# Optimization experiments

Hardware: AMD Instinct MI355X
Metric: run time of the kernel (lower is better)

Reference implementation:

```python
import jax, jax.numpy as jnp
import numpy as np

B = 64          # graphs per batch
MAX_NODES = 512 # nodes per graph
N = B * MAX_NODES
DEG = 16
E = N * DEG
F_IN = 12
H, D = 4, 32    # heads, per-head dim
HID = H * D     # 128
A = 512         # num_outputs (action space)
NEG_SLOPE = 0.2


def setup_inputs() -> dict:
    key = jax.random.key(0)
    ks = jax.random.split(key, 32)
    x = jax.random.normal(ks[0], (N, F_IN), dtype=jnp.float32)
    # edges confined within each graph's node block (as in the torch adjacency loop)
    src_l = jax.random.randint(ks[1], (B, MAX_NODES * DEG), 0, MAX_NODES, dtype=jnp.int32)
    dst_l = jax.random.randint(ks[2], (B, MAX_NODES * DEG), 0, MAX_NODES, dtype=jnp.int32)
    offs = (jnp.arange(B, dtype=jnp.int32) * MAX_NODES)[:, None]
    edge_src = (src_l + offs).reshape(-1)
    edge_dst = (dst_l + offs).reshape(-1)
    batch_idx = jnp.repeat(jnp.arange(B, dtype=jnp.int32), MAX_NODES)

    s = 0.1
    p = {}
    p["Wl0"] = s * jax.random.normal(ks[3], (F_IN, H, D), dtype=jnp.float32)
    p["Wr0"] = s * jax.random.normal(ks[4], (F_IN, H, D), dtype=jnp.float32)
    p["att0"] = s * jax.random.normal(ks[5], (H, D), dtype=jnp.float32)
    p["b0"] = jnp.zeros((HID,), dtype=jnp.float32)
    p["Wl"] = s * jax.random.normal(ks[6], (3, HID, H, D), dtype=jnp.float32)
    p["Wr"] = s * jax.random.normal(ks[7], (3, HID, H, D), dtype=jnp.float32)
    p["att"] = s * jax.random.normal(ks[8], (3, H, D), dtype=jnp.float32)
    p["b"] = jnp.zeros((3, HID), dtype=jnp.float32)
    p["qW1"] = s * jax.random.normal(ks[9], (2 * HID, HID), dtype=jnp.float32)
    p["qb1"] = jnp.zeros((HID,), dtype=jnp.float32)
    p["qW2"] = s * jax.random.normal(ks[10], (HID, A), dtype=jnp.float32)
    p["qb2"] = jnp.zeros((A,), dtype=jnp.float32)
    p["vW1"] = s * jax.random.normal(ks[11], (2 * HID, HID), dtype=jnp.float32)
    p["vb1"] = jnp.zeros((HID,), dtype=jnp.float32)
    p["vW2"] = s * jax.random.normal(ks[12], (HID, 1), dtype=jnp.float32)
    p["vb2"] = jnp.zeros((1,), dtype=jnp.float32)
    return dict(x=x, edge_src=edge_src, edge_dst=edge_dst, batch_idx=batch_idx, **p)


def _gatv2(x, src, dst, Wl, Wr, att, b):
    n = x.shape[0]
    xl = jnp.einsum('nf,fhd->nhd', x, Wl)  # source transform [N,H,D]
    xr = jnp.einsum('nf,fhd->nhd', x, Wr)  # target transform [N,H,D]
    xj = xl[src]                            # [E,H,D]
    e = jax.nn.leaky_relu(xj + xr[dst], NEG_SLOPE)
    s = jnp.einsum('ehd,hd->eh', e, att)    # [E,H]
    smax = jax.ops.segment_max(s, dst, num_segments=n)
    smax = jnp.where(jnp.isfinite(smax), smax, 0.0)
    a = jnp.exp(s - smax[dst])
    den = jax.ops.segment_sum(a, dst, num_segments=n)
    a = a / jnp.maximum(den[dst], 1e-16)
    out = jax.ops.segment_sum(a[:, :, None] * xj, dst, num_segments=n)  # [N,H,D]
    return out.reshape(n, H * D) + b


def reference(x, edge_src, edge_dst, batch_idx,
              Wl0, Wr0, att0, b0, Wl, Wr, att, b,
              qW1, qb1, qW2, qb2, vW1, vb1, vW2, vb2):
    h = jax.nn.relu(_gatv2(x, edge_src, edge_dst, Wl0, Wr0, att0, b0))
    for i in range(3):  # remaining num_layers-1 GATv2 layers (dropout off in eval)
        h = jax.nn.relu(_gatv2(h, edge_src, edge_dst, Wl[i], Wr[i], att[i], b[i]))
    nb = h.shape[0] // MAX_NODES
    gsum = jax.ops.segment_sum(h, batch_idx, num_segments=nb)
    cnt = jax.ops.segment_sum(jnp.ones((h.shape[0], 1), h.dtype), batch_idx, num_segments=nb)
    gmean = gsum / jnp.maximum(cnt, 1.0)
    gmax = jax.ops.segment_max(h, batch_idx, num_segments=nb)
    g = jnp.concatenate([gmean, gmax], axis=-1)  # [B, 2*HID]
    adv = jax.nn.relu(g @ qW1 + qb1) @ qW2 + qb2
    val = jax.nn.relu(g @ vW1 + vb1) @ vW2 + vb2
    q = val + (adv - adv.mean(axis=-1, keepdims=True))
    return q
```

## Files before the change

### kernel.cpp

```cpp
#include <hip/hip_runtime.h>
#include <hip/hip_bf16.h>

#define NN 32768
#define EE 524288
#define HID 128
#define BGRAPH 64
#define MAXN 512
#define AOUT 512
#define MAXDEG 64

typedef __attribute__((ext_vector_type(8))) short short8;
typedef __attribute__((ext_vector_type(4))) float f32x4;
typedef unsigned short ushort;
typedef unsigned int uint;

__device__ __forceinline__ ushort bf16_rn(float f) {
    uint u = __float_as_uint(f);
    u += 0x7FFF + ((u >> 16) & 1);
    return (ushort)(u >> 16);
}
__device__ __forceinline__ void bf16_split(float f, ushort& hi, ushort& lo) {
    hi = bf16_rn(f);
    float fh = __uint_as_float(((uint)hi) << 16);
    lo = bf16_rn(f - fh);
}

__device__ __forceinline__ float vsum4(f32x4 v) {
    return (v.x + v.y) + (v.z + v.w);
}

__global__ __launch_bounds__(256) void setup_kernel(
    const int* __restrict__ src, const int* __restrict__ dst,
    int* __restrict__ cursor, int* __restrict__ bucket,
    const float* __restrict__ Wl, const float* __restrict__ Wr,
    ushort* __restrict__ wt_hi, ushort* __restrict__ wt_lo) {
    int blk = blockIdx.x;
    if (blk < EE / 256) {
        int i = blk * 256 + threadIdx.x;
        int d = dst[i];
        int p = atomicAdd(&cursor[d], 1);
        if (p < MAXDEG) bucket[(size_t)d * MAXDEG + p] = src[i];
    } else {
        int idx = (blk - EE / 256) * 256 + threadIdx.x;
        if (idx >= 98304) return;
        int c = idx & 127;
        int k = (idx >> 7) & 127;
        int l = (idx >> 14) % 3;
        int lr = idx / 49152;
        float v = (lr ? Wr : Wl)[l * 16384 + k * 128 + c];
        ushort hi, lo;
        bf16_split(v, hi, lo);
        int ct = c >> 4, m = c & 15;
        int ks = k >> 5;
        int lane = (((k >> 3) & 3) << 4) | m;
        int j = k & 7;
        size_t o = ((size_t)(lr * 3 + l) * 32 + ct * 4 + ks) * 512 + lane * 8 + j;
        wt_hi[o] = hi;
        wt_lo[o] = lo;
    }
}

template<int KTOT, int KC>
__global__ __launch_bounds__(256) void transform3(
    const float* __restrict__ hin, const float* __restrict__ Wl,
    const float* __restrict__ Wr, float* __restrict__ xl, float* __restrict__ xr) {
    __shared__ float wb[KC][256];
    __shared__ float ha[KC][36];
    int b = blockIdx.x;
    int xcd = b & 7, slot = b >> 3;
    int graph = xcd + 8 * (slot >> 4);
    int chunk = slot & 15;
    int node0 = graph * 512 + chunk * 32;
    int t = threadIdx.x;
    int c32 = t & 31;
    int ng  = t >> 5;
    const float4* wl4g = (const float4*)Wl;
    const float4* wr4g = (const float4*)Wr;
    for (int idx = t; idx < KC * 64; idx += 256) {
        int k = idx >> 6, r = idx & 63;
        float4 v = (r < 32) ? wl4g[k * 32 + r] : wr4g[k * 32 + (r - 32)];
        ((float4*)&wb[k][0])[r] = v;
    }
    for (int idx = t; idx < 32 * KC; idx += 256) {
        int m = idx / KC, kk = idx - m * KC;
        ha[kk][m] = hin[(size_t)(node0 + m) * KTOT + kk];
    }
    __syncthreads();
    float4 accL[4], accR[4];
#pragma unroll
    for (int m = 0; m < 4; m++) {
        accL[m].x = accL[m].y = accL[m].z = accL[m].w = 0.f;
        accR[m].x = accR[m].y = accR[m].z = accR[m].w = 0.f;
    }
#pragma unroll
    for (int kk = 0; kk < KC; kk++) {
        float4 wl = ((const float4*)&wb[kk][0])[c32];
        float4 wr = ((const float4*)&wb[kk][128])[c32];
        float4 hv = *(const float4*)&ha[kk][ng * 4];
        accL[0].x = fmaf(hv.x, wl.x, accL[0].x); accL[0].y = fmaf(hv.x, wl.y, accL[0].y);
        accL[0].z = fmaf(hv.x, wl.z, accL[0].z); accL[0].w = fmaf(hv.x, wl.w, accL[0].w);
        accL[1].x = fmaf(hv.y, wl.x, accL[1].x); accL[1].y = fmaf(hv.y, wl.y, accL[1].y);
        accL[1].z = fmaf(hv.y, wl.z, accL[1].z); accL[1].w = fmaf(hv.y, wl.w, accL[1].w);
        accL[2].x = fmaf(hv.z, wl.x, accL[2].x); accL[2].y = fmaf(hv.z, wl.y, accL[2].y);
        accL[2].z = fmaf(hv.z, wl.z, accL[2].z); accL[2].w = fmaf(hv.z, wl.w, accL[2].w);
        accL[3].x = fmaf(hv.w, wl.x, accL[3].x); accL[3].y = fmaf(hv.w, wl.y, accL[3].y);
        accL[3].z = fmaf(hv.w, wl.z, accL[3].z); accL[3].w = fmaf(hv.w, wl.w, accL[3].w);
        accR[0].x = fmaf(hv.x, wr.x, accR[0].x); accR[0].y = fmaf(hv.x, wr.y, accR[0].y);
        accR[0].z = fmaf(hv.x, wr.z, accR[0].z); accR[0].w = fmaf(hv.x, wr.w, accR[0].w);
        accR[1].x = fmaf(hv.y, wr.x, accR[1].x); accR[1].y = fmaf(hv.y, wr.y, accR[1].y);
        accR[1].z = fmaf(hv.y, wr.z, accR[1].z); accR[1].w = fmaf(hv.y, wr.w, accR[1].w);
        accR[2].x = fmaf(hv.z, wr.x, accR[2].x); accR[2].y = fmaf(hv.z, wr.y, accR[2].y);
        accR[2].z = fmaf(hv.z, wr.z, accR[2].z); accR[2].w = fmaf(hv.z, wr.w, accR[2].w);
        accR[3].x = fmaf(hv.w, wr.x, accR[3].x); accR[3].y = fmaf(hv.w, wr.y, accR[3].y);
        accR[3].z = fmaf(hv.w, wr.z, accR[3].z); accR[3].w = fmaf(hv.w, wr.w, accR[3].w);
    }
    float4* xlo = (float4*)xl;
    float4* xro = (float4*)xr;
#pragma unroll
    for (int m = 0; m < 4; m++) {
        int n = node0 + ng * 4 + m;
        xlo[n * 32 + c32] = accL[m];
        xro[n * 32 + c32] = accR[m];
    }
}

__device__ __forceinline__ void gat_node2_dual(
    const f32x4* __restrict__ xl4, const f32x4* __restrict__ xr4,
    const int* __restrict__ browA, int nEA, int nA,
    const int* __restrict__ browB, int nEB, int nBn,
    int el2, int p16, f32x4 at0, f32x4 at1,
    f32x4& oA0, f32x4& oA1, f32x4& oB0, f32x4& oB1) {
    f32x4 xrA0 = xr4[(size_t)nA * 32 + p16 * 2];
    f32x4 xrA1 = xr4[(size_t)nA * 32 + p16 * 2 + 1];
    f32x4 xrB0 = xr4[(size_t)nBn * 32 + p16 * 2];
    f32x4 xrB1 = xr4[(size_t)nBn * 32 + p16 * 2 + 1];
    f32x4 aA0 = {0.f, 0.f, 0.f, 0.f};
    f32x4 aA1 = {0.f, 0.f, 0.f, 0.f};
    f32x4 aB0 = {0.f, 0.f, 0.f, 0.f};
    f32x4 aB1 = {0.f, 0.f, 0.f, 0.f};
    float denA = 0.f, denB = 0.f;
    int nBlkA = (nEA + 7) >> 3;
    int nBlkB = (nEB + 7) >> 3;
    int nBlk = nBlkA > nBlkB ? nBlkA : nBlkB;
    int4 iA = *(const int4*)(browA + el2 * 4);
    int4 iB = *(const int4*)(browB + el2 * 4);
    for (int blk = 0; blk < nBlk; blk++) {
        int ebase = blk * 8 + el2 * 4;
        int noff = ebase + 8;
        int nmax = MAXDEG - 8 + el2 * 4;
        noff = noff > nmax ? nmax : noff;
        int4 iAn = *(const int4*)(browA + noff);
        int4 iBn = *(const int4*)(browB + noff);

#define LOADC(c, vA0_, vA1_, vB0_, vB1_) {                                        \
        int rawA = (c == 0) ? iA.x : (c == 1) ? iA.y : (c == 2) ? iA.z : iA.w;    \
        int rawB = (c == 0) ? iB.x : (c == 1) ? iB.y : (c == 2) ? iB.z : iB.w;    \
        int e = ebase + c;                                                        \
        int sA = (e < nEA) ? rawA : nA;                                           \
        int sB = (e < nEB) ? rawB : nBn;                                          \
        const f32x4* rA = xl4 + (size_t)sA * 32 + p16 * 2;                        \
        const f32x4* rB = xl4 + (size_t)sB * 32 + p16 * 2;                        \
        vA0_ = rA[0]; vA1_ = rA[1]; vB0_ = rB[0]; vB1_ = rB[1]; }

#define COMPUTEC(c, vA0_, vA1_, vB0_, vB1_) {                                     \
        int e = ebase + c;                                                        \
        f32x4 u, lA0, lA1, lB0, lB1;                                              \
        u = vA0_ + xrA0; lA0 = __builtin_elementwise_max(u, 0.2f * u);            \
        u = vA1_ + xrA1; lA1 = __builtin_elementwise_max(u, 0.2f * u);            \
        u = vB0_ + xrB0; lB0 = __builtin_elementwise_max(u, 0.2f * u);            \
        u = vB1_ + xrB1; lB1 = __builtin_elementwise_max(u, 0.2f * u);            \
        f32x4 tvA = at0 * lA0 + at1 * lA1;                                        \
        f32x4 tvB = at0 * lB0 + at1 * lB1;                                        \
        float tA = vsum4(tvA), tB = vsum4(tvB);                                   \
        tA += __shfl_xor(tA, 1); tA += __shfl_xor(tA, 2);                         \
        tB += __shfl_xor(tB, 1); tB += __shfl_xor(tB, 2);                         \
        float wA = (e < nEA) ? __expf(tA) : 0.f;                                  \
        float wB = (e < nEB) ? __expf(tB) : 0.f;                                  \
        denA += wA; denB += wB;                                                   \
        aA0 += wA * vA0_; aA1 += wA * vA1_;                                       \
        aB0 += wB * vB0_; aB1 += wB * vB1_; }

        f32x4 p0, p1, p2, p3, q0, q1, q2, q3;
        LOADC(0, p0, p1, p2, p3)
        LOADC(1, q0, q1, q2, q3)
        COMPUTEC(0, p0, p1, p2, p3)
        LOADC(2, p0, p1, p2, p3)
        COMPUTEC(1, q0, q1, q2, q3)
        LOADC(3, q0, q1, q2, q3)
        COMPUTEC(2, p0, p1, p2, p3)
        COMPUTEC(3, q0, q1, q2, q3)
#undef LOADC
#undef COMPUTEC
        iA = iAn; iB = iBn;
    }
    aA0.x += __shfl_xor(aA0.x, 16); aA0.y += __shfl_xor(aA0.y, 16);
    aA0.z += __shfl_xor(aA0.z, 16); aA0.w += __shfl_xor(aA0.w, 16);
    aA1.x += __shfl_xor(aA1.x, 16); aA1.y += __shfl_xor(aA1.y, 16);
    aA1.z += __shfl_xor(aA1.z, 16); aA1.w += __shfl_xor(aA1.w, 16);
    aB0.x += __shfl_xor(aB0.x, 16); aB0.y += __shfl_xor(aB0.y, 16);
    aB0.z += __shfl_xor(aB0.z, 16); aB0.w += __shfl_xor(aB0.w, 16);
    aB1.x += __shfl_xor(aB1.x, 16); aB1.y += __shfl_xor(aB1.y, 16);
    aB1.z += __shfl_xor(aB1.z, 16); aB1.w += __shfl_xor(aB1.w, 16);
    denA += __shfl_xor(denA, 16);
    denB += __shfl_xor(denB, 16);
    float rdenA = 1.0f / fmaxf(denA, 1e-16f);
    float rdenB = 1.0f / fmaxf(denB, 1e-16f);
    oA0 = aA0 * rdenA; oA1 = aA1 * rdenA;
    oB0 = aB0 * rdenB; oB1 = aB1 * rdenB;
}

__device__ __forceinline__ f32x4 relu_bias(f32x4 o, f32x4 bv) {
    f32x4 z = {0.f, 0.f, 0.f, 0.f};
    return __builtin_elementwise_max(o + bv, z);
}

__device__ __forceinline__ void store_h(f32x4 o0, f32x4 o1,
                                        ushort (*hh)[136], ushort (*hl)[136],
                                        int nl, int p16) {
    float f[8];
    f[0] = o0.x; f[1] = o0.y; f[2] = o0.z; f[3] = o0.w;
    f[4] = o1.x; f[5] = o1.y; f[6] = o1.z; f[7] = o1.w;
    ushort hi[8], lo[8];
#pragma unroll
    for (int i = 0; i < 8; i++) bf16_split(f[i], hi[i], lo[i]);
    uint4 ph, pl;
    ph.x = (uint)hi[0] | ((uint)hi[1] << 16);
    ph.y = (uint)hi[2] | ((uint)hi[3] << 16);
    ph.z = (uint)hi[4] | ((uint)hi[5] << 16);
    ph.w = (uint)hi[6] | ((uint)hi[7] << 16);
    pl.x = (uint)lo[0] | ((uint)lo[1] << 16);
    pl.y = (uint)lo[2] | ((uint)lo[3] << 16);
    pl.z = (uint)lo[4] | ((uint)lo[5] << 16);
    pl.w = (uint)lo[6] | ((uint)lo[7] << 16);
    *(uint4*)&hh[nl][p16 * 8] = ph;
    *(uint4*)&hl[nl][p16 * 8] = pl;
}

__global__ __launch_bounds__(256, 4) void fused_agg_mfma(
    const float* __restrict__ xl_in, const float* __restrict__ xr_in,
    const int* __restrict__ bucket, const int* __restrict__ cnt,
    const float* __restrict__ att, const float* __restrict__ bias,
    const ushort* __restrict__ wl_hi, const ushort* __restrict__ wl_lo,
    const ushort* __restrict__ wr_hi, const ushort* __restrict__ wr_lo,
    float* __restrict__ xl_out, float* __restrict__ xr_out) {
    __shared__ ushort hh[16][136];
    __shared__ ushort hl[16][136];
    int b = blockIdx.x;
    int xcd = b & 7, slot = b >> 3;
    int graph = xcd + 8 * (slot >> 5);
    int chunk = slot & 31;
    int node_base = graph * 512 + chunk * 16;
    int wid = threadIdx.x >> 6;
    int lane = threadIdx.x & 63;
    int n0 = node_base + wid * 4;
    int nh  = lane >> 5;
    int el2 = (lane >> 4) & 1;
    int p16 = lane & 15;
    {
        const f32x4* xl4 = (const f32x4*)xl_in;
        const f32x4* xr4 = (const f32x4*)xr_in;
        const f32x4* att4 = (const f32x4*)att;
        f32x4 at0 = att4[p16 * 2];
        f32x4 at1 = att4[p16 * 2 + 1];
        int nA  = n0 + nh;
        int nBn = n0 + 2 + nh;
        int nEA = cnt[nA];  nEA = (nEA > MAXDEG) ? MAXDEG : nEA;
        int nEB = cnt[nBn]; nEB = (nEB > MAXDEG) ? MAXDEG : nEB;
        f32x4 oA0, oA1, oB0, oB1;
        gat_node2_dual(xl4, xr4,
                       bucket + (size_t)nA * MAXDEG, nEA, nA,
                       bucket + (size_t)nBn * MAXDEG, nEB, nBn,
                       el2, p16, at0, at1, oA0, oA1, oB0, oB1);
        if (el2 == 0) {
            const f32x4* bias4 = (const f32x4*)bias;
            f32x4 b0v = bias4[p16 * 2];
            f32x4 b1v = bias4[p16 * 2 + 1];
            oA0 = relu_bias(oA0, b0v); oA1 = relu_bias(oA1, b1v);
            oB0 = relu_bias(oB0, b0v); oB1 = relu_bias(oB1, b1v);
            store_h(oA0, oA1, hh, hl, wid * 4 + nh, p16);
            store_h(oB0, oB1, hh, hl, wid * 4 + 2 + nh, p16);
        }
    }
    __syncthreads();
    int m = lane & 15, quad = lane >> 4;
    f32x4 accL[2], accR[2];
#pragma unroll
    for (int c2 = 0; c2 < 2; c2++) {
        accL[c2] = (f32x4){0.f, 0.f, 0.f, 0.f};
        accR[c2] = (f32x4){0.f, 0.f, 0.f, 0.f};
    }
#pragma unroll
    for (int ks = 0; ks < 4; ks++) {
        short8 ah = *(const short8*)&hh[m][ks * 32 + quad * 8];
        short8 al = *(const short8*)&hl[m][ks * 32 + quad * 8];
#pragma unroll
        for (int c2 = 0; c2 < 2; c2++) {
            int ct = wid * 2 + c2;
            size_t wb = ((size_t)(ct * 4 + ks) * 64 + lane) * 8;
            short8 bhl = *(const short8*)(wl_hi + wb);
            short8 bll = *(const short8*)(wl_lo + wb);
            short8 bhr = *(const short8*)(wr_hi + wb);
            short8 blr = *(const short8*)(wr_lo + wb);
            accL[c2] = __builtin_amdgcn_mfma_f32_16x16x32_bf16(ah, bhl, accL[c2], 0, 0, 0);
            accL[c2] = __builtin_amdgcn_mfma_f32_16x16x32_bf16(ah, bll, accL[c2], 0, 0, 0);
            accL[c2] = __builtin_amdgcn_mfma_f32_16x16x32_bf16(al, bhl, accL[c2], 0, 0, 0);
            accR[c2] = __builtin_amdgcn_mfma_f32_16x16x32_bf16(ah, bhr, accR[c2], 0, 0, 0);
            accR[c2] = __builtin_amdgcn_mfma_f32_16x16x32_bf16(ah, blr, accR[c2], 0, 0, 0);
            accR[c2] = __builtin_amdgcn_mfma_f32_16x16x32_bf16(al, bhr, accR[c2], 0, 0, 0);
        }
    }
#pragma unroll
    for (int c2 = 0; c2 < 2; c2++) {
        int ct = wid * 2 + c2;
#pragma unroll
        for (int r = 0; r < 4; r++) {
            int node = node_base + quad * 4 + r;
            xl_out[(size_t)node * 128 + ct * 16 + m] = accL[c2][r];
            xr_out[(size_t)node * 128 + ct * 16 + m] = accR[c2][r];
        }
    }
}

__global__ __launch_bounds__(256, 4) void agg_pool(
    const float* __restrict__ xl_in, const float* __restrict__ xr_in,
    const int* __restrict__ bucket, const int* __restrict__ cnt,
    const float* __restrict__ att, const float* __restrict__ bias,
    float* __restrict__ psum, float* __restrict__ pmax) {
    __shared__ float sums[4][128];
    __shared__ float maxs[4][128];
    int b = blockIdx.x;
    int xcd = b & 7, slot = b >> 3;
    int graph = xcd + 8 * (slot >> 5);
    int chunk = slot & 31;
    int wid = threadIdx.x >> 6;
    int lane = threadIdx.x & 63;
    int n0 = graph * 512 + chunk * 16 + wid * 4;
    int nh  = lane >> 5;
    int el2 = (lane >> 4) & 1;
    int p16 = lane & 15;
    const f32x4* xl4 = (const f32x4*)xl_in;
    const f32x4* xr4 = (const f32x4*)xr_in;
    const f32x4* att4 = (const f32x4*)att;
    const f32x4* bias4 = (const f32x4*)bias;
    f32x4 at0 = att4[p16 * 2];
    f32x4 at1 = att4[p16 * 2 + 1];
    f32x4 b0v = bias4[p16 * 2];
    f32x4 b1v = bias4[p16 * 2 + 1];
    int nA  = n0 + nh;
    int nBn = n0 + 2 + nh;
    int nEA = cnt[nA];  nEA = (nEA > MAXDEG) ? MAXDEG : nEA;
    int nEB = cnt[nBn]; nEB = (nEB > MAXDEG) ? MAXDEG : nEB;
    f32x4 oA0, oA1, oB0, oB1;
    gat_node2_dual(xl4, xr4,
                   bucket + (size_t)nA * MAXDEG, nEA, nA,
                   bucket + (size_t)nBn * MAXDEG, nEB, nBn,
                   el2, p16, at0, at1, oA0, oA1, oB0, oB1);
    oA0 = relu_bias(oA0, b0v); oA1 = relu_bias(oA1, b1v);
    oB0 = relu_bias(oB0, b0v); oB1 = relu_bias(oB1, b1v);
    f32x4 s0 = oA0 + oB0;
    f32x4 s1 = oA1 + oB1;
    f32x4 m0 = __builtin_elementwise_max(oA0, oB0);
    f32x4 m1 = __builtin_elementwise_max(oA1, oB1);
    s0.x += __shfl_xor(s0.x, 32); s0.y += __shfl_xor(s0.y, 32);
    s0.z += __shfl_xor(s0.z, 32); s0.w += __shfl_xor(s0.w, 32);
    s1.x += __shfl_xor(s1.x, 32); s1.y += __shfl_xor(s1.y, 32);
    s1.z += __shfl_xor(s1.z, 32); s1.w += __shfl_xor(s1.w, 32);
    m0.x = fmaxf(m0.x, __shfl_xor(m0.x, 32)); m0.y = fmaxf(m0.y, __shfl_xor(m0.y, 32));
    m0.z = fmaxf(m0.z, __shfl_xor(m0.z, 32)); m0.w = fmaxf(m0.w, __shfl_xor(m0.w, 32));
    m1.x = fmaxf(m1.x, __shfl_xor(m1.x, 32)); m1.y = fmaxf(m1.y, __shfl_xor(m1.y, 32));
    m1.z = fmaxf(m1.z, __shfl_xor(m1.z, 32)); m1.w = fmaxf(m1.w, __shfl_xor(m1.w, 32));
    if (nh == 0 && el2 == 0) {
        *(f32x4*)&sums[wid][p16 * 8]     = s0;
        *(f32x4*)&sums[wid][p16 * 8 + 4] = s1;
        *(f32x4*)&maxs[wid][p16 * 8]     = m0;
        *(f32x4*)&maxs[wid][p16 * 8 + 4] = m1;
    }
    __syncthreads();
    int t = threadIdx.x;
    if (t < 128) {
        float s = 0.f, m = -1e30f;
#pragma unroll
        for (int ww = 0; ww < 4; ww++) {
            s += sums[ww][t];
            m = fmaxf(m, maxs[ww][t]);
        }
        psum[((size_t)graph * 32 + chunk) * 128 + t] = s;
        pmax[((size_t)graph * 32 + chunk) * 128 + t] = m;
    }
}

__global__ __launch_bounds__(512) void head_kernel(
    const float* __restrict__ psum, const float* __restrict__ pmax,
    const float* __restrict__ qW1, const float* __restrict__ qb1,
    const float* __restrict__ qW2, const float* __restrict__ qb2,
    const float* __restrict__ vW1, const float* __restrict__ vb1,
    const float* __restrict__ vW2, const float* __restrict__ vb2,
    float* __restrict__ qout) {
    __shared__ float gs[256];
    __shared__ float hq[128];
    __shared__ float hv[128];
    __shared__ float red[512];
    int b = blockIdx.x, t = threadIdx.x;
    if (t < 128) {
        float s = 0.f, m = -1e30f;
#pragma unroll 8
        for (int c = 0; c < 32; c++) {
            s += psum[((size_t)b * 32 + c) * 128 + t];
            m = fmaxf(m, pmax[((size_t)b * 32 + c) * 128 + t]);
        }
        gs[t] = s * (1.0f / 512.0f);
        gs[128 + t] = m;
    }
    __syncthreads();
    if (t < 128) {
        float acc = qb1[t];
        for (int k = 0; k < 256; k++) acc = fmaf(gs[k], qW1[k * 128 + t], acc);
        hq[t] = fmaxf(acc, 0.f);
    } else if (t < 256) {
        int tt = t - 128;
        float acc = vb1[tt];
        for (int k = 0; k < 256; k++) acc = fmaf(gs[k], vW1[k * 128 + tt], acc);
        hv[tt] = fmaxf(acc, 0.f);
    }
    __syncthreads();
    float adv = qb2[t];
    for (int k = 0; k < 128; k++) adv = fmaf(hq[k], qW2[k * 512 + t], adv);
    red[t] = (t < 128) ? hv[t] * vW2[t] : 0.f;
    __syncthreads();
    for (int off = 256; off > 0; off >>= 1) {
        if (t < off) red[t] += red[t + off];
        __syncthreads();
    }
    float val = red[0] + vb2[0];
    __syncthreads();
    red[t] = adv;
    __syncthreads();
    for (int off = 256; off > 0; off >>= 1) {
        if (t < off) red[t] += red[t + off];
        __syncthreads();
    }
    float mean_adv = red[0] * (1.0f / 512.0f);
    qout[b * 512 + t] = val + adv - mean_adv;
}

extern "C" void kernel_launch(void* const* d_in, const int* in_sizes, int n_in,
                              void* d_out, int out_size, void* d_ws, size_t ws_size,
                              hipStream_t stream) {
    const float* x        = (const float*)d_in[0];
    const int* edge_src   = (const int*)d_in[1];
    const int* edge_dst   = (const int*)d_in[2];
    const float* Wl0 = (const float*)d_in[4];
    const float* Wr0 = (const float*)d_in[5];
    const float* att0 = (const float*)d_in[6];
    const float* b0 = (const float*)d_in[7];
    const float* Wl = (const float*)d_in[8];
    const float* Wr = (const float*)d_in[9];
    const float* att = (const float*)d_in[10];
    const float* bb = (const float*)d_in[11];
    const float* qW1 = (const float*)d_in[12];
    const float* qb1 = (const float*)d_in[13];
    const float* qW2 = (const float*)d_in[14];
    const float* qb2 = (const float*)d_in[15];
    const float* vW1 = (const float*)d_in[16];
    const float* vb1 = (const float*)d_in[17];
    const float* vW2 = (const float*)d_in[18];
    const float* vb2 = (const float*)d_in[19];

    int* cursor  = (int*)d_ws;
    int* bucket  = cursor + NN;
    float* fbase = (float*)(bucket + (size_t)NN * MAXDEG);
    float* xlA   = fbase;
    float* xrA   = xlA + NN * 128;
    float* xlB   = xrA + NN * 128;
    float* xrB   = xlB + NN * 128;
    float* psum  = xrB + NN * 128;
    float* pmax  = psum + BGRAPH * 32 * 128;
    ushort* wthi = (ushort*)(pmax + BGRAPH * 32 * 128);
    ushort* wtlo = wthi + 2 * 3 * 16384;

    hipMemsetAsync(cursor, 0, NN * sizeof(int), stream);
    setup_kernel<<<EE / 256 + 384, 256, 0, stream>>>(edge_src, edge_dst, cursor, bucket,
                                                     Wl, Wr, wthi, wtlo);

    transform3<12, 12><<<NN / 32, 256, 0, stream>>>(x, Wl0, Wr0, xlA, xrA);

    fused_agg_mfma<<<NN / 16, 256, 0, stream>>>(xlA, xrA, bucket, cursor, att0, b0,
                                                wthi + 0 * 16384, wtlo + 0 * 16384,
                                                wthi + 3 * 16384, wtlo + 3 * 16384,
                                                xlB, xrB);
    fused_agg_mfma<<<NN / 16, 256, 0, stream>>>(xlB, xrB, bucket, cursor, att, bb,
                                                wthi + 1 * 16384, wtlo + 1 * 16384,
                                                wthi + 4 * 16384, wtlo + 4 * 16384,
                                                xlA, xrA);
    fused_agg_mfma<<<NN / 16, 256, 0, stream>>>(xlA, xrA, bucket, cursor,
                                                att + 128, bb + 128,
                                                wthi + 2 * 16384, wtlo + 2 * 16384,
                                                wthi + 5 * 16384, wtlo + 5 * 16384,
                                                xlB, xrB);
    agg_pool<<<NN / 16, 256, 0, stream>>>(xlB, xrB, bucket, cursor,
                                          att + 256, bb + 256, psum, pmax);
    head_kernel<<<BGRAPH, 512, 0, stream>>>(psum, pmax, qW1, qb1, qW2, qb2,
                                            vW1, vb1, vW2, vb2, (float*)d_out);
}
```

Before: 271.3 us.

## Split each node's edge list across four lane groups with 512-thread blocks

Each wave now aggregates two nodes instead of four, and the 64 lanes split each node's edges into four interleaved groups of 4 (16 edges per iteration) instead of two. Blocks grow to 512 threads (8 waves per 16 nodes), and each wave in the MFMA projection handles one 16-column tile instead of two. The aim is more memory-level parallelism and shorter per-wave edge loops for the gather-bound aggregation. The cost is an extra cross-lane reduction step, more padding waste for low-degree nodes with 16-edge blocks, and higher register pressure under launch_bounds(512,4).

```diff
diff --git a/kernel.cpp b/kernel.cpp
--- a/kernel.cpp
+++ b/kernel.cpp
@@ -128,7 +128,7 @@
     const f32x4* __restrict__ xl4, const f32x4* __restrict__ xr4,
     const int* __restrict__ browA, int nEA, int nA,
     const int* __restrict__ browB, int nEB, int nBn,
-    int el2, int p16, f32x4 at0, f32x4 at1,
+    int el4, int p16, f32x4 at0, f32x4 at1,
     f32x4& oA0, f32x4& oA1, f32x4& oB0, f32x4& oB1) {
     f32x4 xrA0 = xr4[(size_t)nA * 32 + p16 * 2];
     f32x4 xrA1 = xr4[(size_t)nA * 32 + p16 * 2 + 1];
@@ -139,15 +139,14 @@
     f32x4 aB0 = {0.f, 0.f, 0.f, 0.f};
     f32x4 aB1 = {0.f, 0.f, 0.f, 0.f};
     float denA = 0.f, denB = 0.f;
-    int nBlkA = (nEA + 7) >> 3;
-    int nBlkB = (nEB + 7) >> 3;
-    int nBlk = nBlkA > nBlkB ? nBlkA : nBlkB;
-    int4 iA = *(const int4*)(browA + el2 * 4);
-    int4 iB = *(const int4*)(browB + el2 * 4);
+    int nEmax = nEA > nEB ? nEA : nEB;
+    int nBlk = (nEmax + 15) >> 4;
+    int4 iA = *(const int4*)(browA + el4 * 4);
+    int4 iB = *(const int4*)(browB + el4 * 4);
     for (int blk = 0; blk < nBlk; blk++) {
-        int ebase = blk * 8 + el2 * 4;
-        int noff = ebase + 8;
-        int nmax = MAXDEG - 8 + el2 * 4;
+        int ebase = blk * 16 + el4 * 4;
+        int noff = ebase + 16;
+        int nmax = (MAXDEG - 16) + el4 * 4;
         noff = noff > nmax ? nmax : noff;
         int4 iAn = *(const int4*)(browA + noff);
         int4 iBn = *(const int4*)(browB + noff);
@@ -193,16 +192,17 @@
 #undef COMPUTEC
         iA = iAn; iB = iBn;
     }
-    aA0.x += __shfl_xor(aA0.x, 16); aA0.y += __shfl_xor(aA0.y, 16);
-    aA0.z += __shfl_xor(aA0.z, 16); aA0.w += __shfl_xor(aA0.w, 16);
-    aA1.x += __shfl_xor(aA1.x, 16); aA1.y += __shfl_xor(aA1.y, 16);
-    aA1.z += __shfl_xor(aA1.z, 16); aA1.w += __shfl_xor(aA1.w, 16);
-    aB0.x += __shfl_xor(aB0.x, 16); aB0.y += __shfl_xor(aB0.y, 16);
-    aB0.z += __shfl_xor(aB0.z, 16); aB0.w += __shfl_xor(aB0.w, 16);
-    aB1.x += __shfl_xor(aB1.x, 16); aB1.y += __shfl_xor(aB1.y, 16);
-    aB1.z += __shfl_xor(aB1.z, 16); aB1.w += __shfl_xor(aB1.w, 16);
+#define RED16_32(v) \
+    v.x += __shfl_xor(v.x, 16); v.y += __shfl_xor(v.y, 16);                      \
+    v.z += __shfl_xor(v.z, 16); v.w += __shfl_xor(v.w, 16);                      \
+    v.x += __shfl_xor(v.x, 32); v.y += __shfl_xor(v.y, 32);                      \
+    v.z += __shfl_xor(v.z, 32); v.w += __shfl_xor(v.w, 32);
+    RED16_32(aA0) RED16_32(aA1) RED16_32(aB0) RED16_32(aB1)
+#undef RED16_32
     denA += __shfl_xor(denA, 16);
+    denA += __shfl_xor(denA, 32);
     denB += __shfl_xor(denB, 16);
+    denB += __shfl_xor(denB, 32);
     float rdenA = 1.0f / fmaxf(denA, 1e-16f);
     float rdenB = 1.0f / fmaxf(denB, 1e-16f);
     oA0 = aA0 * rdenA; oA1 = aA1 * rdenA;
@@ -236,7 +236,7 @@
     *(uint4*)&hl[nl][p16 * 8] = pl;
 }
 
-__global__ __launch_bounds__(256, 4) void fused_agg_mfma(
+__global__ __launch_bounds__(512, 4) void fused_agg_mfma(
     const float* __restrict__ xl_in, const float* __restrict__ xr_in,
     const int* __restrict__ bucket, const int* __restrict__ cnt,
     const float* __restrict__ att, const float* __restrict__ bias,
@@ -252,9 +252,7 @@
     int node_base = graph * 512 + chunk * 16;
     int wid = threadIdx.x >> 6;
     int lane = threadIdx.x & 63;
-    int n0 = node_base + wid * 4;
-    int nh  = lane >> 5;
-    int el2 = (lane >> 4) & 1;
+    int el4 = (lane >> 4) & 3;
     int p16 = lane & 15;
     {
         const f32x4* xl4 = (const f32x4*)xl_in;
@@ -262,81 +260,68 @@
         const f32x4* att4 = (const f32x4*)att;
         f32x4 at0 = att4[p16 * 2];
         f32x4 at1 = att4[p16 * 2 + 1];
-        int nA  = n0 + nh;
-        int nBn = n0 + 2 + nh;
+        int nA  = node_base + wid * 2;
+        int nBn = node_base + wid * 2 + 1;
         int nEA = cnt[nA];  nEA = (nEA > MAXDEG) ? MAXDEG : nEA;
         int nEB = cnt[nBn]; nEB = (nEB > MAXDEG) ? MAXDEG : nEB;
         f32x4 oA0, oA1, oB0, oB1;
         gat_node2_dual(xl4, xr4,
                        bucket + (size_t)nA * MAXDEG, nEA, nA,
                        bucket + (size_t)nBn * MAXDEG, nEB, nBn,
-                       el2, p16, at0, at1, oA0, oA1, oB0, oB1);
-        if (el2 == 0) {
+                       el4, p16, at0, at1, oA0, oA1, oB0, oB1);
+        if (el4 == 0) {
             const f32x4* bias4 = (const f32x4*)bias;
             f32x4 b0v = bias4[p16 * 2];
             f32x4 b1v = bias4[p16 * 2 + 1];
             oA0 = relu_bias(oA0, b0v); oA1 = relu_bias(oA1, b1v);
             oB0 = relu_bias(oB0, b0v); oB1 = relu_bias(oB1, b1v);
-            store_h(oA0, oA1, hh, hl, wid * 4 + nh, p16);
-            store_h(oB0, oB1, hh, hl, wid * 4 + 2 + nh, p16);
+            store_h(oA0, oA1, hh, hl, wid * 2, p16);
+            store_h(oB0, oB1, hh, hl, wid * 2 + 1, p16);
         }
     }
     __syncthreads();
     int m = lane & 15, quad = lane >> 4;
-    f32x4 accL[2], accR[2];
-#pragma unroll
-    for (int c2 = 0; c2 < 2; c2++) {
-        accL[c2] = (f32x4){0.f, 0.f, 0.f, 0.f};
-        accR[c2] = (f32x4){0.f, 0.f, 0.f, 0.f};
-    }
+    f32x4 accL = {0.f, 0.f, 0.f, 0.f};
+    f32x4 accR = {0.f, 0.f, 0.f, 0.f};
+    int ct = wid;
 #pragma unroll
     for (int ks = 0; ks < 4; ks++) {
         short8 ah = *(const short8*)&hh[m][ks * 32 + quad * 8];
         short8 al = *(const short8*)&hl[m][ks * 32 + quad * 8];
-#pragma unroll
-        for (int c2 = 0; c2 < 2; c2++) {
-            int ct = wid * 2 + c2;
-            size_t wb = ((size_t)(ct * 4 + ks) * 64 + lane) * 8;
-            short8 bhl = *(const short8*)(wl_hi + wb);
-            short8 bll = *(const short8*)(wl_lo + wb);
-            short8 bhr = *(const short8*)(wr_hi + wb);
-            short8 blr = *(const short8*)(wr_lo + wb);
-            accL[c2] = __builtin_amdgcn_mfma_f32_16x16x32_bf16(ah, bhl, accL[c2], 0, 0, 0);
-            accL[c2] = __builtin_amdgcn_mfma_f32_16x16x32_bf16(ah, bll, accL[c2], 0, 0, 0);
-            accL[c2] = __builtin_amdgcn_mfma_f32_16x16x32_bf16(al, bhl, accL[c2], 0, 0, 0);
-            accR[c2] = __builtin_amdgcn_mfma_f32_16x16x32_bf16(ah, bhr, accR[c2], 0, 0, 0);
-            accR[c2] = __builtin_amdgcn_mfma_f32_16x16x32_bf16(ah, blr, accR[c2], 0, 0, 0);
-            accR[c2] = __builtin_amdgcn_mfma_f32_16x16x32_bf16(al, bhr, accR[c2], 0, 0, 0);
-        }
-    }
-#pragma unroll
-    for (int c2 = 0; c2 < 2; c2++) {
-        int ct = wid * 2 + c2;
-#pragma unroll
-        for (int r = 0; r < 4; r++) {
-            int node = node_base + quad * 4 + r;
-            xl_out[(size_t)node * 128 + ct * 16 + m] = accL[c2][r];
-            xr_out[(size_t)node * 128 + ct * 16 + m] = accR[c2][r];
-        }
-    }
-}
-
-__global__ __launch_bounds__(256, 4) void agg_pool(
+        size_t wb = ((size_t)(ct * 4 + ks) * 64 + lane) * 8;
+        short8 bhl = *(const short8*)(wl_hi + wb);
+        short8 bll = *(const short8*)(wl_lo + wb);
+        short8 bhr = *(const short8*)(wr_hi + wb);
+        short8 blr = *(const short8*)(wr_lo + wb);
+        accL = __builtin_amdgcn_mfma_f32_16x16x32_bf16(ah, bhl, accL, 0, 0, 0);
+        accL = __builtin_amdgcn_mfma_f32_16x16x32_bf16(ah, bll, accL, 0, 0, 0);
+        accL = __builtin_amdgcn_mfma_f32_16x16x32_bf16(al, bhl, accL, 0, 0, 0);
+        accR = __builtin_amdgcn_mfma_f32_16x16x32_bf16(ah, bhr, accR, 0, 0, 0);
+        accR = __builtin_amdgcn_mfma_f32_16x16x32_bf16(ah, blr, accR, 0, 0, 0);
+        accR = __builtin_amdgcn_mfma_f32_16x16x32_bf16(al, bhr, accR, 0, 0, 0);
+    }
+#pragma unroll
+    for (int r = 0; r < 4; r++) {
+        int node = node_base + quad * 4 + r;
+        xl_out[(size_t)node * 128 + ct * 16 + m] = accL[r];
+        xr_out[(size_t)node * 128 + ct * 16 + m] = accR[r];
+    }
+}
+
+__global__ __launch_bounds__(512, 4) void agg_pool(
     const float* __restrict__ xl_in, const float* __restrict__ xr_in,
     const int* __restrict__ bucket, const int* __restrict__ cnt,
     const float* __restrict__ att, const float* __restrict__ bias,
     float* __restrict__ psum, float* __restrict__ pmax) {
-    __shared__ float sums[4][128];
-    __shared__ float maxs[4][128];
+    __shared__ float sums[8][128];
+    __shared__ float maxs[8][128];
     int b = blockIdx.x;
     int xcd = b & 7, slot = b >> 3;
     int graph = xcd + 8 * (slot >> 5);
     int chunk = slot & 31;
     int wid = threadIdx.x >> 6;
     int lane = threadIdx.x & 63;
-    int n0 = graph * 512 + chunk * 16 + wid * 4;
-    int nh  = lane >> 5;
-    int el2 = (lane >> 4) & 1;
+    int el4 = (lane >> 4) & 3;
     int p16 = lane & 15;
     const f32x4* xl4 = (const f32x4*)xl_in;
     const f32x4* xr4 = (const f32x4*)xr_in;
@@ -346,30 +331,23 @@
     f32x4 at1 = att4[p16 * 2 + 1];
     f32x4 b0v = bias4[p16 * 2];
     f32x4 b1v = bias4[p16 * 2 + 1];
-    int nA  = n0 + nh;
-    int nBn = n0 + 2 + nh;
+    int node_base = graph * 512 + chunk * 16;
+    int nA  = node_base + wid * 2;
+    int nBn = node_base + wid * 2 + 1;
     int nEA = cnt[nA];  nEA = (nEA > MAXDEG) ? MAXDEG : nEA;
     int nEB = cnt[nBn]; nEB = (nEB > MAXDEG) ? MAXDEG : nEB;
     f32x4 oA0, oA1, oB0, oB1;
     gat_node2_dual(xl4, xr4,
                    bucket + (size_t)nA * MAXDEG, nEA, nA,
                    bucket + (size_t)nBn * MAXDEG, nEB, nBn,
-                   el2, p16, at0, at1, oA0, oA1, oB0, oB1);
+                   el4, p16, at0, at1, oA0, oA1, oB0, oB1);
     oA0 = relu_bias(oA0, b0v); oA1 = relu_bias(oA1, b1v);
     oB0 = relu_bias(oB0, b0v); oB1 = relu_bias(oB1, b1v);
     f32x4 s0 = oA0 + oB0;
     f32x4 s1 = oA1 + oB1;
     f32x4 m0 = __builtin_elementwise_max(oA0, oB0);
     f32x4 m1 = __builtin_elementwise_max(oA1, oB1);
-    s0.x += __shfl_xor(s0.x, 32); s0.y += __shfl_xor(s0.y, 32);
-    s0.z += __shfl_xor(s0.z, 32); s0.w += __shfl_xor(s0.w, 32);
-    s1.x += __shfl_xor(s1.x, 32); s1.y += __shfl_xor(s1.y, 32);
-    s1.z += __shfl_xor(s1.z, 32); s1.w += __shfl_xor(s1.w, 32);
-    m0.x = fmaxf(m0.x, __shfl_xor(m0.x, 32)); m0.y = fmaxf(m0.y, __shfl_xor(m0.y, 32));
-    m0.z = fmaxf(m0.z, __shfl_xor(m0.z, 32)); m0.w = fmaxf(m0.w, __shfl_xor(m0.w, 32));
-    m1.x = fmaxf(m1.x, __shfl_xor(m1.x, 32)); m1.y = fmaxf(m1.y, __shfl_xor(m1.y, 32));
-    m1.z = fmaxf(m1.z, __shfl_xor(m1.z, 32)); m1.w = fmaxf(m1.w, __shfl_xor(m1.w, 32));
-    if (nh == 0 && el2 == 0) {
+    if (el4 == 0) {
         *(f32x4*)&sums[wid][p16 * 8]     = s0;
         *(f32x4*)&sums[wid][p16 * 8 + 4] = s1;
         *(f32x4*)&maxs[wid][p16 * 8]     = m0;
@@ -380,7 +358,7 @@
     if (t < 128) {
         float s = 0.f, m = -1e30f;
 #pragma unroll
-        for (int ww = 0; ww < 4; ww++) {
+        for (int ww = 0; ww < 8; ww++) {
             s += sums[ww][t];
             m = fmaxf(m, maxs[ww][t]);
         }
@@ -484,20 +462,20 @@
 
     transform3<12, 12><<<NN / 32, 256, 0, stream>>>(x, Wl0, Wr0, xlA, xrA);
 
-    fused_agg_mfma<<<NN / 16, 256, 0, stream>>>(xlA, xrA, bucket, cursor, att0, b0,
+    fused_agg_mfma<<<NN / 16, 512, 0, stream>>>(xlA, xrA, bucket, cursor, att0, b0,
                                                 wthi + 0 * 16384, wtlo + 0 * 16384,
                                                 wthi + 3 * 16384, wtlo + 3 * 16384,
                                                 xlB, xrB);
-    fused_agg_mfma<<<NN / 16, 256, 0, stream>>>(xlB, xrB, bucket, cursor, att, bb,
+    fused_agg_mfma<<<NN / 16, 512, 0, stream>>>(xlB, xrB, bucket, cursor, att, bb,
                                                 wthi + 1 * 16384, wtlo + 1 * 16384,
                                                 wthi + 4 * 16384, wtlo + 4 * 16384,
                                                 xlA, xrA);
-    fused_agg_mfma<<<NN / 16, 256, 0, stream>>>(xlA, xrA, bucket, cursor,
+    fused_agg_mfma<<<NN / 16, 512, 0, stream>>>(xlA, xrA, bucket, cursor,
                                                 att + 128, bb + 128,
                                                 wthi + 2 * 16384, wtlo + 2 * 16384,
                                                 wthi + 5 * 16384, wtlo + 5 * 16384,
                                                 xlB, xrB);
-    agg_pool<<<NN / 16, 256, 0, stream>>>(xlB, xrB, bucket, cursor,
+    agg_pool<<<NN / 16, 512, 0, stream>>>(xlB, xrB, bucket, cursor,
                                           att + 256, bb + 256, psum, pmax);
     head_kernel<<<BGRAPH, 512, 0, stream>>>(psum, pmax, qW1, qb1, qW2, qb2,
                                             vW1, vb1, vW2, vb2, (float*)d_out);
```

Result: slower. 287.6 us (+6.0%).

## Process one node per wave with four edge lanes instead of dual-node pairs

Applied to the files above, without the earlier changes.

Replaces the dual-node aggregation, where each wave handled two node pairs with two edge slots, with a per-node loop in which all 64 lanes work on one node at a time: four edge groups of 16 lanes, with a one-ahead prefetch of the next gathered row. Each wave now loops serially over its four nodes. The aim is to cut wasted iterations when degrees differ between paired nodes (the old loop ran to the max of the two) and to lower register pressure. The trade-off is less memory-level parallelism per wave, since fewer independent gathers are in flight and the node loop is serialized.

```diff
diff --git a/kernel.cpp b/kernel.cpp
--- a/kernel.cpp
+++ b/kernel.cpp
@@ -124,89 +124,55 @@
     }
 }
 
-__device__ __forceinline__ void gat_node2_dual(
-    const f32x4* __restrict__ xl4, const f32x4* __restrict__ xr4,
-    const int* __restrict__ browA, int nEA, int nA,
-    const int* __restrict__ browB, int nEB, int nBn,
-    int el2, int p16, f32x4 at0, f32x4 at1,
-    f32x4& oA0, f32x4& oA1, f32x4& oB0, f32x4& oB1) {
-    f32x4 xrA0 = xr4[(size_t)nA * 32 + p16 * 2];
-    f32x4 xrA1 = xr4[(size_t)nA * 32 + p16 * 2 + 1];
-    f32x4 xrB0 = xr4[(size_t)nBn * 32 + p16 * 2];
-    f32x4 xrB1 = xr4[(size_t)nBn * 32 + p16 * 2 + 1];
-    f32x4 aA0 = {0.f, 0.f, 0.f, 0.f};
-    f32x4 aA1 = {0.f, 0.f, 0.f, 0.f};
-    f32x4 aB0 = {0.f, 0.f, 0.f, 0.f};
-    f32x4 aB1 = {0.f, 0.f, 0.f, 0.f};
-    float denA = 0.f, denB = 0.f;
-    int nBlkA = (nEA + 7) >> 3;
-    int nBlkB = (nEB + 7) >> 3;
-    int nBlk = nBlkA > nBlkB ? nBlkA : nBlkB;
-    int4 iA = *(const int4*)(browA + el2 * 4);
-    int4 iB = *(const int4*)(browB + el2 * 4);
-    for (int blk = 0; blk < nBlk; blk++) {
-        int ebase = blk * 8 + el2 * 4;
-        int noff = ebase + 8;
-        int nmax = MAXDEG - 8 + el2 * 4;
-        noff = noff > nmax ? nmax : noff;
-        int4 iAn = *(const int4*)(browA + noff);
-        int4 iBn = *(const int4*)(browB + noff);
-
-#define LOADC(c, vA0_, vA1_, vB0_, vB1_) {                                        \
-        int rawA = (c == 0) ? iA.x : (c == 1) ? iA.y : (c == 2) ? iA.z : iA.w;    \
-        int rawB = (c == 0) ? iB.x : (c == 1) ? iB.y : (c == 2) ? iB.z : iB.w;    \
-        int e = ebase + c;                                                        \
-        int sA = (e < nEA) ? rawA : nA;                                           \
-        int sB = (e < nEB) ? rawB : nBn;                                          \
-        const f32x4* rA = xl4 + (size_t)sA * 32 + p16 * 2;                        \
-        const f32x4* rB = xl4 + (size_t)sB * 32 + p16 * 2;                        \
-        vA0_ = rA[0]; vA1_ = rA[1]; vB0_ = rB[0]; vB1_ = rB[1]; }
-
-#define COMPUTEC(c, vA0_, vA1_, vB0_, vB1_) {                                     \
-        int e = ebase + c;                                                        \
-        f32x4 u, lA0, lA1, lB0, lB1;                                              \
-        u = vA0_ + xrA0; lA0 = __builtin_elementwise_max(u, 0.2f * u);            \
-        u = vA1_ + xrA1; lA1 = __builtin_elementwise_max(u, 0.2f * u);            \
-        u = vB0_ + xrB0; lB0 = __builtin_elementwise_max(u, 0.2f * u);            \
-        u = vB1_ + xrB1; lB1 = __builtin_elementwise_max(u, 0.2f * u);            \
-        f32x4 tvA = at0 * lA0 + at1 * lA1;                                        \
-        f32x4 tvB = at0 * lB0 + at1 * lB1;                                        \
-        float tA = vsum4(tvA), tB = vsum4(tvB);                                   \
-        tA += __shfl_xor(tA, 1); tA += __shfl_xor(tA, 2);                         \
-        tB += __shfl_xor(tB, 1); tB += __shfl_xor(tB, 2);                         \
-        float wA = (e < nEA) ? __expf(tA) : 0.f;                                  \
-        float wB = (e < nEB) ? __expf(tB) : 0.f;                                  \
-        denA += wA; denB += wB;                                                   \
-        aA0 += wA * vA0_; aA1 += wA * vA1_;                                       \
-        aB0 += wB * vB0_; aB1 += wB * vB1_; }
-
-        f32x4 p0, p1, p2, p3, q0, q1, q2, q3;
-        LOADC(0, p0, p1, p2, p3)
-        LOADC(1, q0, q1, q2, q3)
-        COMPUTEC(0, p0, p1, p2, p3)
-        LOADC(2, p0, p1, p2, p3)
-        COMPUTEC(1, q0, q1, q2, q3)
-        LOADC(3, q0, q1, q2, q3)
-        COMPUTEC(2, p0, p1, p2, p3)
-        COMPUTEC(3, q0, q1, q2, q3)
-#undef LOADC
-#undef COMPUTEC
-        iA = iAn; iB = iBn;
-    }
-    aA0.x += __shfl_xor(aA0.x, 16); aA0.y += __shfl_xor(aA0.y, 16);
-    aA0.z += __shfl_xor(aA0.z, 16); aA0.w += __shfl_xor(aA0.w, 16);
-    aA1.x += __shfl_xor(aA1.x, 16); aA1.y += __shfl_xor(aA1.y, 16);
-    aA1.z += __shfl_xor(aA1.z, 16); aA1.w += __shfl_xor(aA1.w, 16);
-    aB0.x += __shfl_xor(aB0.x, 16); aB0.y += __shfl_xor(aB0.y, 16);
-    aB0.z += __shfl_xor(aB0.z, 16); aB0.w += __shfl_xor(aB0.w, 16);
-    aB1.x += __shfl_xor(aB1.x, 16); aB1.y += __shfl_xor(aB1.y, 16);
-    aB1.z += __shfl_xor(aB1.z, 16); aB1.w += __shfl_xor(aB1.w, 16);
-    denA += __shfl_xor(denA, 16);
-    denB += __shfl_xor(denB, 16);
-    float rdenA = 1.0f / fmaxf(denA, 1e-16f);
-    float rdenB = 1.0f / fmaxf(denB, 1e-16f);
-    oA0 = aA0 * rdenA; oA1 = aA1 * rdenA;
-    oB0 = aB0 * rdenB; oB1 = aB1 * rdenB;
+__device__ __forceinline__ void gat_node_one(
+    const f32x4* __restrict__ xl4, const int* __restrict__ brow,
+    int nE, int n, f32x4 xr0, f32x4 xr1,
+    int el4, int p16, f32x4 at0, f32x4 at1,
+    f32x4& o0, f32x4& o1) {
+    f32x4 a0 = {0.f, 0.f, 0.f, 0.f};
+    f32x4 a1 = {0.f, 0.f, 0.f, 0.f};
+    float den = 0.f;
+    int nB = (nE + 3) >> 2;
+    int e = el4;
+    int s0i = (e < nE) ? brow[e] : n;
+    const f32x4* r0 = xl4 + (size_t)s0i * 32 + p16 * 2;
+    f32x4 cv0 = r0[0], cv1 = r0[1];
+    for (int blk = 0; blk < nB; blk++) {
+        f32x4 pv0, pv1;
+        if (blk + 1 < nB) {
+            int en = e + 4;
+            int eni = en > (MAXDEG - 1) ? (MAXDEG - 1) : en;
+            int sn = (en < nE) ? brow[eni] : n;
+            const f32x4* rn = xl4 + (size_t)sn * 32 + p16 * 2;
+            pv0 = rn[0]; pv1 = rn[1];
+        }
+        f32x4 u0 = cv0 + xr0;
+        f32x4 u1 = cv1 + xr1;
+        f32x4 l0 = __builtin_elementwise_max(u0, 0.2f * u0);
+        f32x4 l1 = __builtin_elementwise_max(u1, 0.2f * u1);
+        f32x4 tv = at0 * l0 + at1 * l1;
+        float t = vsum4(tv);
+        t += __shfl_xor(t, 1);
+        t += __shfl_xor(t, 2);
+        float a = (e < nE) ? __expf(t) : 0.f;
+        den += a;
+        a0 += a * cv0;
+        a1 += a * cv1;
+        if (blk + 1 < nB) { cv0 = pv0; cv1 = pv1; }
+        e += 4;
+    }
+#define RED2(v) \
+    v.x += __shfl_xor(v.x, 16); v.y += __shfl_xor(v.y, 16);                      \
+    v.z += __shfl_xor(v.z, 16); v.w += __shfl_xor(v.w, 16);                      \
+    v.x += __shfl_xor(v.x, 32); v.y += __shfl_xor(v.y, 32);                      \
+    v.z += __shfl_xor(v.z, 32); v.w += __shfl_xor(v.w, 32);
+    RED2(a0) RED2(a1)
+#undef RED2
+    den += __shfl_xor(den, 16);
+    den += __shfl_xor(den, 32);
+    float rden = 1.0f / fmaxf(den, 1e-16f);
+    o0 = a0 * rden;
+    o1 = a1 * rden;
 }
 
 __device__ __forceinline__ f32x4 relu_bias(f32x4 o, f32x4 bv) {
@@ -252,33 +218,39 @@
     int node_base = graph * 512 + chunk * 16;
     int wid = threadIdx.x >> 6;
     int lane = threadIdx.x & 63;
-    int n0 = node_base + wid * 4;
-    int nh  = lane >> 5;
-    int el2 = (lane >> 4) & 1;
+    int el4 = (lane >> 4) & 3;
     int p16 = lane & 15;
     {
         const f32x4* xl4 = (const f32x4*)xl_in;
         const f32x4* xr4 = (const f32x4*)xr_in;
         const f32x4* att4 = (const f32x4*)att;
+        const f32x4* bias4 = (const f32x4*)bias;
         f32x4 at0 = att4[p16 * 2];
         f32x4 at1 = att4[p16 * 2 + 1];
-        int nA  = n0 + nh;
-        int nBn = n0 + 2 + nh;
-        int nEA = cnt[nA];  nEA = (nEA > MAXDEG) ? MAXDEG : nEA;
-        int nEB = cnt[nBn]; nEB = (nEB > MAXDEG) ? MAXDEG : nEB;
-        f32x4 oA0, oA1, oB0, oB1;
-        gat_node2_dual(xl4, xr4,
-                       bucket + (size_t)nA * MAXDEG, nEA, nA,
-                       bucket + (size_t)nBn * MAXDEG, nEB, nBn,
-                       el2, p16, at0, at1, oA0, oA1, oB0, oB1);
-        if (el2 == 0) {
-            const f32x4* bias4 = (const f32x4*)bias;
-            f32x4 b0v = bias4[p16 * 2];
-            f32x4 b1v = bias4[p16 * 2 + 1];
-            oA0 = relu_bias(oA0, b0v); oA1 = relu_bias(oA1, b1v);
-            oB0 = relu_bias(oB0, b0v); oB1 = relu_bias(oB1, b1v);
-            store_h(oA0, oA1, hh, hl, wid * 4 + nh, p16);
-            store_h(oB0, oB1, hh, hl, wid * 4 + 2 + nh, p16);
+        f32x4 b0v = bias4[p16 * 2];
+        f32x4 b1v = bias4[p16 * 2 + 1];
+        int n0 = node_base + wid * 4;
+        int nE[4];
+        f32x4 xr0[4], xr1[4];
+#pragma unroll
+        for (int i = 0; i < 4; i++) {
+            int n = n0 + i;
+            int d = cnt[n];
+            nE[i] = (d > MAXDEG) ? MAXDEG : d;
+            xr0[i] = xr4[(size_t)n * 32 + p16 * 2];
+            xr1[i] = xr4[(size_t)n * 32 + p16 * 2 + 1];
+        }
+#pragma unroll 1
+        for (int i = 0; i < 4; i++) {
+            int n = n0 + i;
+            f32x4 o0, o1;
+            gat_node_one(xl4, bucket + (size_t)n * MAXDEG, nE[i], n,
+                         xr0[i], xr1[i], el4, p16, at0, at1, o0, o1);
+            if (el4 == 0) {
+                o0 = relu_bias(o0, b0v);
+                o1 = relu_bias(o1, b1v);
+                store_h(o0, o1, hh, hl, wid * 4 + i, p16);
+            }
         }
     }
     __syncthreads();
@@ -334,9 +306,7 @@
     int chunk = slot & 31;
     int wid = threadIdx.x >> 6;
     int lane = threadIdx.x & 63;
-    int n0 = graph * 512 + chunk * 16 + wid * 4;
-    int nh  = lane >> 5;
-    int el2 = (lane >> 4) & 1;
+    int el4 = (lane >> 4) & 3;
     int p16 = lane & 15;
     const f32x4* xl4 = (const f32x4*)xl_in;
     const f32x4* xr4 = (const f32x4*)xr_in;
@@ -346,30 +316,35 @@
     f32x4 at1 = att4[p16 * 2 + 1];
     f32x4 b0v = bias4[p16 * 2];
     f32x4 b1v = bias4[p16 * 2 + 1];
-    int nA  = n0 + nh;
-    int nBn = n0 + 2 + nh;
-    int nEA = cnt[nA];  nEA = (nEA > MAXDEG) ? MAXDEG : nEA;
-    int nEB = cnt[nBn]; nEB = (nEB > MAXDEG) ? MAXDEG : nEB;
-    f32x4 oA0, oA1, oB0, oB1;
-    gat_node2_dual(xl4, xr4,
-                   bucket + (size_t)nA * MAXDEG, nEA, nA,
-                   bucket + (size_t)nBn * MAXDEG, nEB, nBn,
-                   el2, p16, at0, at1, oA0, oA1, oB0, oB1);
-    oA0 = relu_bias(oA0, b0v); oA1 = relu_bias(oA1, b1v);
-    oB0 = relu_bias(oB0, b0v); oB1 = relu_bias(oB1, b1v);
-    f32x4 s0 = oA0 + oB0;
-    f32x4 s1 = oA1 + oB1;
-    f32x4 m0 = __builtin_elementwise_max(oA0, oB0);
-    f32x4 m1 = __builtin_elementwise_max(oA1, oB1);
-    s0.x += __shfl_xor(s0.x, 32); s0.y += __shfl_xor(s0.y, 32);
-    s0.z += __shfl_xor(s0.z, 32); s0.w += __shfl_xor(s0.w, 32);
-    s1.x += __shfl_xor(s1.x, 32); s1.y += __shfl_xor(s1.y, 32);
-    s1.z += __shfl_xor(s1.z, 32); s1.w += __shfl_xor(s1.w, 32);
-    m0.x = fmaxf(m0.x, __shfl_xor(m0.x, 32)); m0.y = fmaxf(m0.y, __shfl_xor(m0.y, 32));
-    m0.z = fmaxf(m0.z, __shfl_xor(m0.z, 32)); m0.w = fmaxf(m0.w, __shfl_xor(m0.w, 32));
-    m1.x = fmaxf(m1.x, __shfl_xor(m1.x, 32)); m1.y = fmaxf(m1.y, __shfl_xor(m1.y, 32));
-    m1.z = fmaxf(m1.z, __shfl_xor(m1.z, 32)); m1.w = fmaxf(m1.w, __shfl_xor(m1.w, 32));
-    if (nh == 0 && el2 == 0) {
+    int node_base = graph * 512 + chunk * 16;
+    int n0 = node_base + wid * 4;
+    int nE[4];
+    f32x4 xr0[4], xr1[4];
+#pragma unroll
+    for (int i = 0; i < 4; i++) {
+        int n = n0 + i;
+        int d = cnt[n];
+        nE[i] = (d > MAXDEG) ? MAXDEG : d;
+        xr0[i] = xr4[(size_t)n * 32 + p16 * 2];
+        xr1[i] = xr4[(size_t)n * 32 + p16 * 2 + 1];
+    }
+    f32x4 s0 = {0.f, 0.f, 0.f, 0.f};
+    f32x4 s1 = {0.f, 0.f, 0.f, 0.f};
+    f32x4 m0 = {-1e30f, -1e30f, -1e30f, -1e30f};
+    f32x4 m1 = {-1e30f, -1e30f, -1e30f, -1e30f};
+#pragma unroll 1
+    for (int i = 0; i < 4; i++) {
+        int n = n0 + i;
+        f32x4 o0, o1;
+        gat_node_one(xl4, bucket + (size_t)n * MAXDEG, nE[i], n,
+                     xr0[i], xr1[i], el4, p16, at0, at1, o0, o1);
+        o0 = relu_bias(o0, b0v);
+        o1 = relu_bias(o1, b1v);
+        s0 += o0; s1 += o1;
+        m0 = __builtin_elementwise_max(m0, o0);
+        m1 = __builtin_elementwise_max(m1, o1);
+    }
+    if (el4 == 0) {
         *(f32x4*)&sums[wid][p16 * 8]     = s0;
         *(f32x4*)&sums[wid][p16 * 8 + 4] = s1;
         *(f32x4*)&maxs[wid][p16 * 8]     = m0;
```

Result: slower. 314.6 us (+16.0%).
